# Performance work log

Hardware: AMD Instinct MI355X
Metric: run time of the kernel (lower is better)

Reference implementation:

```python
import jax, jax.numpy as jnp
import numpy as np

ALPHA = 0.8  # LeakyReLU negative slope
OUT_DIM = 128
EDGE_DIM = 64


def setup_inputs() -> dict:
    key = jax.random.key(0)
    ks = jax.random.split(key, 6)
    N, NS, IN, OUT, ED = 25000, 32, 128, OUT_DIM, EDGE_DIM
    return {
        "input": jax.random.normal(ks[0], (N, IN), jnp.float32),
        "neigh_feat": jax.random.normal(ks[1], (N * NS, IN), jnp.float32),
        "edge_emb": jax.random.normal(ks[2], (N * NS, ED), jnp.float32),
        "mask": jnp.zeros((N,), jnp.int32),  # unused by forward, kept for signature fidelity
        "W": jax.random.normal(ks[3], (IN, OUT), jnp.float32) * 0.1,
        "W2": jax.random.normal(ks[4], (IN, OUT), jnp.float32) * 0.1,
        "a": jax.random.normal(ks[5], (2 * OUT + ED, 1), jnp.float32) * 0.1,
    }


def reference(input, neigh_feat, edge_emb, mask, W, W2, a):
    N = input.shape[0]
    ns = neigh_feat.shape[0] // N
    out_dim = W.shape[1]
    ed = edge_emb.shape[1]

    x = input @ W                                   # [N, out]
    neighs = (neigh_feat @ W2).reshape(N, ns, out_dim)  # [N, ns, out]
    edge = edge_emb.reshape(N, ns, ed)              # [N, ns, ed]

    # a_input @ a decomposed: avoid materializing the repeated/concatenated tensor.
    a_x = a[:out_dim, 0]
    a_n = a[out_dim:2 * out_dim, 0]
    a_e = a[2 * out_dim:, 0]
    scores = (x @ a_x)[:, None] + neighs @ a_n + edge @ a_e  # [N, ns]
    e = jnp.where(scores > 0, scores, ALPHA * scores)        # LeakyReLU(alpha)

    attention = jax.nn.softmax(e, axis=1)           # softmax over neighbors
    # dropout p=0.0 (eval) -> identity

    h_prime = jnp.einsum("ns,nsd->nd", attention, neighs)  # [N, out]
    output = jnp.concatenate([x, h_prime], axis=1)          # concat_node
    e_agg = jnp.einsum("ns,nse->ne", attention, edge)       # concat_edge
    output = jnp.concatenate([output, e_agg], axis=1)       # [N, 2*out+ed]
    return jax.nn.elu(output)
```

## Files before the change

kernel.cpp:

```cpp
#include <hip/hip_runtime.h>
#include <hip/hip_bf16.h>
#include <math.h>

typedef __bf16 bf16_t;
typedef __attribute__((ext_vector_type(8))) __bf16 bf16x8;
typedef __attribute__((ext_vector_type(4))) __bf16 bf16x4;
typedef __attribute__((ext_vector_type(4))) float f32x4;

#define NB 2

#define WAVE_BARRIER() do {                                    \
    asm volatile("s_waitcnt lgkmcnt(0)" ::: "memory");         \
    __builtin_amdgcn_s_barrier();                              \
  } while (0)

__global__ __launch_bounds__(256) void pack_weights_kernel(
    const float* __restrict__ W, const float* __restrict__ W2,
    const float* __restrict__ a,
    bf16_t* __restrict__ Wp, bf16_t* __restrict__ W2p,
    float* __restrict__ w2an, float* __restrict__ wax) {
  int idx = blockIdx.x * 256 + threadIdx.x;
  int j  = idx & 7;
  int l  = (idx >> 3) & 63;
  int nt = (idx >> 9) & 7;
  int kt = idx >> 12;
  int k   = kt * 32 + (l >> 4) * 8 + j;
  int col = nt * 16 + (l & 15);
  Wp[idx]  = (bf16_t)W[k * 128 + col];
  W2p[idx] = (bf16_t)W2[k * 128 + col];
  if (blockIdx.x == 0 && threadIdx.x < 128) {
    const float* r = W2 + threadIdx.x * 128;
    float s = 0.f;
    for (int c = 0; c < 128; ++c) s += r[c] * a[128 + c];
    w2an[threadIdx.x] = s;
  }
  if (blockIdx.x == 1 && threadIdx.x < 128) {
    const float* r = W + threadIdx.x * 128;
    float s = 0.f;
    for (int c = 0; c < 128; ++c) s += r[c] * a[c];
    wax[threadIdx.x] = s;
  }
}

__global__ __launch_bounds__(256, 4) void node_kernel(
    const float* __restrict__ input,
    const float* __restrict__ neigh_feat, const float* __restrict__ edge_emb,
    const float* __restrict__ a, const float* __restrict__ w2an,
    const float* __restrict__ wax,
    const bf16_t* __restrict__ Wp, const bf16_t* __restrict__ W2p,
    float* __restrict__ out) {
  const int t = threadIdx.x;
  const int w = t >> 6, l = t & 63;
  const int n0 = blockIdx.x * NB;

  __shared__ __align__(16) bf16_t AxAh[16 * 128];
  __shared__ float Agg[NB][128];
  __shared__ float srow[32], se[32];
  __shared__ __align__(16) f32x4 nag[4][32];
  __shared__ __align__(16) f32x4 eag[4][16];
  __shared__ float sxs[8];

  const int q = l & 31;
  const int h = l >> 5;
  const int p = l & 15;
  const int g = l >> 4;

  const f32x4 wn = *(const f32x4*)(w2an + 4 * q);
  const f32x4 ae = *(const f32x4*)(a + 256 + 4 * p);

  f32x4 nA[4], eA[2], nB[4], eB[2];

#define ISSUE(P, node_) do {                                              \
    const float* nf_ = neigh_feat + (size_t)(node_) * 4096 + 4 * t;       \
    n##P[0] = __builtin_nontemporal_load((const f32x4*)(nf_));            \
    n##P[1] = __builtin_nontemporal_load((const f32x4*)(nf_ + 1024));     \
    n##P[2] = __builtin_nontemporal_load((const f32x4*)(nf_ + 2048));     \
    n##P[3] = __builtin_nontemporal_load((const f32x4*)(nf_ + 3072));     \
    const float* ee_ = edge_emb + (size_t)(node_) * 2048 + 4 * t;         \
    e##P[0] = __builtin_nontemporal_load((const f32x4*)(ee_));            \
    e##P[1] = __builtin_nontemporal_load((const f32x4*)(ee_ + 1024));     \
  } while (0)

  ISSUE(A, n0);
  ISSUE(B, n0 + 1);

  {
    const int r2 = t >> 5;
    const int c0 = 4 * (t & 31);
    f32x4 iv = {0.f, 0.f, 0.f, 0.f};
    if (r2 < NB) iv = *(const f32x4*)(input + (size_t)(n0 + r2) * 128 + c0);
    f32x4 wv = *(const f32x4*)(wax + c0);
    float s = iv[0]*wv[0] + iv[1]*wv[1] + iv[2]*wv[2] + iv[3]*wv[3];
    s += __shfl_xor(s, 1);  s += __shfl_xor(s, 2);  s += __shfl_xor(s, 4);
    s += __shfl_xor(s, 8);  s += __shfl_xor(s, 16);
    if ((l & 31) == 0) sxs[r2] = s;
    bf16x4 b;
#pragma unroll
    for (int j = 0; j < 4; ++j) b[j] = (bf16_t)iv[j];
    const int gg = (t & 31) >> 1;
    *(bf16x4*)(&AxAh[r2 * 128 + ((gg ^ r2) << 3) + 4 * (t & 1)]) = b;
    bf16x4 z = {(bf16_t)0.f, (bf16_t)0.f, (bf16_t)0.f, (bf16_t)0.f};
    *(bf16x4*)(&AxAh[1024 + 4 * t]) = z;
  }
  __syncthreads();

  {
    const int arow = l & 15;
    f32x4 acc0 = {}, acc1 = {};
#pragma unroll
    for (int kt = 0; kt < 4; ++kt) {
      bf16x8 af = *(const bf16x8*)(&AxAh[arow * 128 + ((kt * 32 + (l >> 4) * 8) ^ ((arow & 7) << 3))]);
      bf16x8 b0 = *(const bf16x8*)(&Wp[((kt * 8 + 2 * w) * 64 + l) * 8]);
      bf16x8 b1 = *(const bf16x8*)(&Wp[((kt * 8 + 2 * w + 1) * 64 + l) * 8]);
      acc0 = __builtin_amdgcn_mfma_f32_16x16x32_bf16(af, b0, acc0, 0, 0, 0);
      acc1 = __builtin_amdgcn_mfma_f32_16x16x32_bf16(af, b1, acc1, 0, 0, 0);
    }
    if ((l >> 4) < 2) {
#pragma unroll
      for (int j = 0; j < 4; ++j) {
        int row = (l >> 4) * 4 + j;
        if (row < NB) {
          float v0 = acc0[j];
          v0 = v0 > 0.f ? v0 : __expf(v0) - 1.f;
          __builtin_nontemporal_store(v0, out + (size_t)(n0 + row) * 320 + 2 * w * 16 + (l & 15));
          float v1 = acc1[j];
          v1 = v1 > 0.f ? v1 : __expf(v1) - 1.f;
          __builtin_nontemporal_store(v1, out + (size_t)(n0 + row) * 320 + (2 * w + 1) * 16 + (l & 15));
        }
      }
    }
  }

#define BODY(P, kk) do {                                                  \
    const int node = n0 + (kk);                                           \
    _Pragma("unroll")                                                     \
    for (int j = 0; j < 4; ++j) {                                         \
      float s = n##P[j][0]*wn[0] + n##P[j][1]*wn[1]                       \
              + n##P[j][2]*wn[2] + n##P[j][3]*wn[3];                      \
      s += __shfl_xor(s, 1);  s += __shfl_xor(s, 2);                      \
      s += __shfl_xor(s, 4);  s += __shfl_xor(s, 8);                      \
      s += __shfl_xor(s, 16);                                             \
      if (q == 0) srow[8*j + 2*w + h] = s;                                \
    }                                                                     \
    _Pragma("unroll")                                                     \
    for (int j = 0; j < 2; ++j) {                                         \
      float s = e##P[j][0]*ae[0] + e##P[j][1]*ae[1]                       \
              + e##P[j][2]*ae[2] + e##P[j][3]*ae[3];                      \
      s += __shfl_xor(s, 1);  s += __shfl_xor(s, 2);                      \
      s += __shfl_xor(s, 4);  s += __shfl_xor(s, 8);                      \
      if (p == 0) se[16*j + 4*w + g] = s;                                 \
    }                                                                     \
    WAVE_BARRIER();                                                       \
    float av;                                                             \
    {                                                                     \
      float e0 = srow[q] + se[q] + sxs[kk];                               \
      e0 = e0 > 0.f ? e0 : 0.8f * e0;                                     \
       \
      float pe = __expf(e0);                                              \
      float s2 = pe;                                                      \
      s2 += __shfl_xor(s2, 1);                                            \
      s2 += __shfl_xor(s2, 2);                                            \
      s2 += __shfl_xor(s2, 4);                                            \
      s2 += __shfl_xor(s2, 8);                                            \
      s2 += __shfl_xor(s2, 16);                                           \
      av = pe / s2;                                                       \
    }                                                                     \
    {                                                                     \
      f32x4 pn = {0.f, 0.f, 0.f, 0.f};                                    \
      _Pragma("unroll")                                                   \
      for (int j = 0; j < 4; ++j) {                                       \
        float as = __shfl(av, 8*j + 2*w + h);                             \
        pn += as * n##P[j];                                               \
      }                                                                   \
      pn[0] += __shfl_xor(pn[0], 32);                                     \
      pn[1] += __shfl_xor(pn[1], 32);                                     \
      pn[2] += __shfl_xor(pn[2], 32);                                     \
      pn[3] += __shfl_xor(pn[3], 32);                                     \
      if (h == 0) nag[w][q] = pn;                                         \
      f32x4 pv = {0.f, 0.f, 0.f, 0.f};                                    \
      _Pragma("unroll")                                                   \
      for (int j = 0; j < 2; ++j) {                                       \
        float as = __shfl(av, 16*j + 4*w + g);                            \
        pv += as * e##P[j];                                               \
      }                                                                   \
      pv[0] += __shfl_xor(pv[0], 16);                                     \
      pv[1] += __shfl_xor(pv[1], 16);                                     \
      pv[2] += __shfl_xor(pv[2], 16);                                     \
      pv[3] += __shfl_xor(pv[3], 16);                                     \
      pv[0] += __shfl_xor(pv[0], 32);                                     \
      pv[1] += __shfl_xor(pv[1], 32);                                     \
      pv[2] += __shfl_xor(pv[2], 32);                                     \
      pv[3] += __shfl_xor(pv[3], 32);                                     \
      if (l < 16) eag[w][p] = pv;                                         \
    }                                                                     \
    WAVE_BARRIER();                                                       \
    if (t < 128) {                                                        \
      const float* f = (const float*)nag;                                 \
      Agg[kk][t] = f[t] + f[128 + t] + f[256 + t] + f[384 + t];           \
    } else if (t < 192) {                                                 \
      int c = t - 128;                                                    \
      const float* f = (const float*)eag;                                 \
      float v = f[c] + f[64 + c] + f[128 + c] + f[192 + c];               \
      v = v > 0.f ? v : __expf(v) - 1.f;                                  \
      __builtin_nontemporal_store(v, out + (size_t)node * 320 + 256 + c); \
    }                                                                     \
  } while (0)

  BODY(A, 0);
  BODY(B, 1);
#undef BODY
#undef ISSUE

  __syncthreads();

  {
    const int r2 = t >> 5;
    const int c0 = 4 * (t & 31);
    f32x4 v = {0.f, 0.f, 0.f, 0.f};
    if (r2 < NB) v = *(const f32x4*)(&Agg[r2][c0]);
    bf16x4 b;
#pragma unroll
    for (int j = 0; j < 4; ++j) b[j] = (bf16_t)v[j];
    const int gg = (t & 31) >> 1;
    *(bf16x4*)(&AxAh[r2 * 128 + ((gg ^ r2) << 3) + 4 * (t & 1)]) = b;
  }
  __syncthreads();
  {
    const int arow = l & 15;
    f32x4 acc0 = {}, acc1 = {};
#pragma unroll
    for (int kt = 0; kt < 4; ++kt) {
      bf16x8 af = *(const bf16x8*)(&AxAh[arow * 128 + ((kt * 32 + (l >> 4) * 8) ^ ((arow & 7) << 3))]);
      bf16x8 b0 = *(const bf16x8*)(&W2p[((kt * 8 + 2 * w) * 64 + l) * 8]);
      bf16x8 b1 = *(const bf16x8*)(&W2p[((kt * 8 + 2 * w + 1) * 64 + l) * 8]);
      acc0 = __builtin_amdgcn_mfma_f32_16x16x32_bf16(af, b0, acc0, 0, 0, 0);
      acc1 = __builtin_amdgcn_mfma_f32_16x16x32_bf16(af, b1, acc1, 0, 0, 0);
    }
    if ((l >> 4) < 2) {
#pragma unroll
      for (int j = 0; j < 4; ++j) {
        int row = (l >> 4) * 4 + j;
        if (row < NB) {
          float v0 = acc0[j];
          v0 = v0 > 0.f ? v0 : __expf(v0) - 1.f;
          __builtin_nontemporal_store(v0, out + (size_t)(n0 + row) * 320 + 128 + 2 * w * 16 + (l & 15));
          float v1 = acc1[j];
          v1 = v1 > 0.f ? v1 : __expf(v1) - 1.f;
          __builtin_nontemporal_store(v1, out + (size_t)(n0 + row) * 320 + 128 + (2 * w + 1) * 16 + (l & 15));
        }
      }
    }
  }
}

extern "C" void kernel_launch(void* const* d_in, const int* in_sizes, int n_in,
                              void* d_out, int out_size, void* d_ws, size_t ws_size,
                              hipStream_t stream) {
  const float* input = (const float*)d_in[0];
  const float* neigh = (const float*)d_in[1];
  const float* edge  = (const float*)d_in[2];
  const float* W     = (const float*)d_in[4];
  const float* W2    = (const float*)d_in[5];
  const float* a     = (const float*)d_in[6];
  float* out = (float*)d_out;

  const int N = in_sizes[0] / 128;

  bf16_t* W2p  = (bf16_t*)d_ws;
  bf16_t* Wp   = W2p + 16384;
  float*  w2an = (float*)((char*)d_ws + 65536);
  float*  wax  = (float*)((char*)d_ws + 66048);

  pack_weights_kernel<<<64, 256, 0, stream>>>(W, W2, a, Wp, W2p, w2an, wax);
  node_kernel<<<N / NB, 256, 0, stream>>>(input, neigh, edge, a, w2an, wax,
                                          Wp, W2p, out);
}
```

Baseline: 143.1 us.

## Compute attention scores and aggregations with MFMA via LDS transpose reads

Replaces the shuffle-based dot products for neighbor and edge scores with bf16 MFMA against a weight vector placed in one column. Neighbor and edge features are converted to bf16 and staged in LDS, and the attention-weighted aggregation is done by MFMA using ds_read_b64_tr_b16 transposed reads. The aim is to remove the many cross-lane shuffles and the LDS reduction stage. In exchange it adds LDS traffic and bf16 rounding of the score and aggregation inputs, which lowers accuracy.

```diff
diff --git a/kernel.cpp b/kernel.cpp
--- a/kernel.cpp
+++ b/kernel.cpp
@@ -52,33 +52,60 @@
   const int t = threadIdx.x;
   const int w = t >> 6, l = t & 63;
   const int n0 = blockIdx.x * NB;
+  const int lr = l & 15;
+  const int lg = l >> 4;
+  const int half = w >> 1;
+  const int mt = w & 1;
+  const int mrow = mt * 16 + lr;
 
   __shared__ __align__(16) bf16_t AxAh[16 * 128];
+  __shared__ __align__(16) bf16_t NFs[4096];
+  __shared__ __align__(16) bf16_t Es[2048];
   __shared__ float Agg[NB][128];
-  __shared__ float srow[32], se[32];
-  __shared__ __align__(16) f32x4 nag[4][32];
-  __shared__ __align__(16) f32x4 eag[4][16];
+  __shared__ float srp[2][32], sep[2][32];
   __shared__ float sxs[8];
 
-  const int q = l & 31;
-  const int h = l >> 5;
-  const int p = l & 15;
-  const int g = l >> 4;
-
-  const f32x4 wn = *(const f32x4*)(w2an + 4 * q);
-  const f32x4 ae = *(const f32x4*)(a + 256 + 4 * p);
-
-  f32x4 nA[4], eA[2], nB[4], eB[2];
-
-#define ISSUE(P, node_) do {                                              \
-    const float* nf_ = neigh_feat + (size_t)(node_) * 4096 + 4 * t;       \
-    n##P[0] = __builtin_nontemporal_load((const f32x4*)(nf_));            \
-    n##P[1] = __builtin_nontemporal_load((const f32x4*)(nf_ + 1024));     \
-    n##P[2] = __builtin_nontemporal_load((const f32x4*)(nf_ + 2048));     \
-    n##P[3] = __builtin_nontemporal_load((const f32x4*)(nf_ + 3072));     \
-    const float* ee_ = edge_emb + (size_t)(node_) * 2048 + 4 * t;         \
-    e##P[0] = __builtin_nontemporal_load((const f32x4*)(ee_));            \
-    e##P[1] = __builtin_nontemporal_load((const f32x4*)(ee_ + 1024));     \
+  bf16x8 bw0, bw1, be;
+  {
+    const float* ws = w2an + half * 64 + lg * 8;
+    f32x4 u0 = *(const f32x4*)(ws);
+    f32x4 u1 = *(const f32x4*)(ws + 4);
+    f32x4 u2 = *(const f32x4*)(ws + 32);
+    f32x4 u3 = *(const f32x4*)(ws + 36);
+    const float* es = a + 256 + half * 32 + lg * 8;
+    f32x4 u4 = *(const f32x4*)(es);
+    f32x4 u5 = *(const f32x4*)(es + 4);
+#pragma unroll
+    for (int j = 0; j < 4; ++j) {
+      bw0[j]   = lr == 0 ? (bf16_t)u0[j] : (bf16_t)0.f;
+      bw0[j+4] = lr == 0 ? (bf16_t)u1[j] : (bf16_t)0.f;
+      bw1[j]   = lr == 0 ? (bf16_t)u2[j] : (bf16_t)0.f;
+      bw1[j+4] = lr == 0 ? (bf16_t)u3[j] : (bf16_t)0.f;
+      be[j]    = lr == 0 ? (bf16_t)u4[j] : (bf16_t)0.f;
+      be[j+4]  = lr == 0 ? (bf16_t)u5[j] : (bf16_t)0.f;
+    }
+  }
+
+  const int posm = (((mrow >> 2) & 1) << 2) | (mrow >> 3);
+  const int c0 = half * 64 + lg * 8;
+  const int c1 = c0 + 32;
+  const int ce = half * 32 + lg * 8;
+  const int wr0 = ((c0 >> 4) * 8 + posm) * 64 + (mrow & 3) * 16 + (c0 & 15);
+  const int wr1 = ((c1 >> 4) * 8 + posm) * 64 + (mrow & 3) * 16 + (c1 & 15);
+  const int wre = ((ce >> 4) * 8 + posm) * 64 + (mrow & 3) * 16 + (ce & 15);
+
+  f32x4 sA0, sA1, sA2, sA3, sA4, sA5;
+  f32x4 sB0, sB1, sB2, sB3, sB4, sB5;
+
+#define ISSUE(P, node_) do {                                                   \
+    const float* nf_ = neigh_feat + (size_t)(node_) * 4096 + mrow * 128 + c0;  \
+    s##P##0 = __builtin_nontemporal_load((const f32x4*)(nf_));                 \
+    s##P##1 = __builtin_nontemporal_load((const f32x4*)(nf_ + 4));             \
+    s##P##2 = __builtin_nontemporal_load((const f32x4*)(nf_ + 32));            \
+    s##P##3 = __builtin_nontemporal_load((const f32x4*)(nf_ + 36));            \
+    const float* ee_ = edge_emb + (size_t)(node_) * 2048 + mrow * 64 + ce;     \
+    s##P##4 = __builtin_nontemporal_load((const f32x4*)(ee_));                 \
+    s##P##5 = __builtin_nontemporal_load((const f32x4*)(ee_ + 4));             \
   } while (0)
 
   ISSUE(A, n0);
@@ -86,10 +113,10 @@
 
   {
     const int r2 = t >> 5;
-    const int c0 = 4 * (t & 31);
+    const int c0p = 4 * (t & 31);
     f32x4 iv = {0.f, 0.f, 0.f, 0.f};
-    if (r2 < NB) iv = *(const f32x4*)(input + (size_t)(n0 + r2) * 128 + c0);
-    f32x4 wv = *(const f32x4*)(wax + c0);
+    if (r2 < NB) iv = *(const f32x4*)(input + (size_t)(n0 + r2) * 128 + c0p);
+    f32x4 wv = *(const f32x4*)(wax + c0p);
     float s = iv[0]*wv[0] + iv[1]*wv[1] + iv[2]*wv[2] + iv[3]*wv[3];
     s += __shfl_xor(s, 1);  s += __shfl_xor(s, 2);  s += __shfl_xor(s, 4);
     s += __shfl_xor(s, 8);  s += __shfl_xor(s, 16);
@@ -105,105 +132,109 @@
   __syncthreads();
 
   {
-    const int arow = l & 15;
     f32x4 acc0 = {}, acc1 = {};
 #pragma unroll
     for (int kt = 0; kt < 4; ++kt) {
-      bf16x8 af = *(const bf16x8*)(&AxAh[arow * 128 + ((kt * 32 + (l >> 4) * 8) ^ ((arow & 7) << 3))]);
+      bf16x8 af = *(const bf16x8*)(&AxAh[lr * 128 + ((kt * 32 + lg * 8) ^ ((lr & 7) << 3))]);
       bf16x8 b0 = *(const bf16x8*)(&Wp[((kt * 8 + 2 * w) * 64 + l) * 8]);
       bf16x8 b1 = *(const bf16x8*)(&Wp[((kt * 8 + 2 * w + 1) * 64 + l) * 8]);
       acc0 = __builtin_amdgcn_mfma_f32_16x16x32_bf16(af, b0, acc0, 0, 0, 0);
       acc1 = __builtin_amdgcn_mfma_f32_16x16x32_bf16(af, b1, acc1, 0, 0, 0);
     }
-    if ((l >> 4) < 2) {
+    if (lg < 2) {
 #pragma unroll
       for (int j = 0; j < 4; ++j) {
-        int row = (l >> 4) * 4 + j;
+        int row = lg * 4 + j;
         if (row < NB) {
           float v0 = acc0[j];
           v0 = v0 > 0.f ? v0 : __expf(v0) - 1.f;
-          __builtin_nontemporal_store(v0, out + (size_t)(n0 + row) * 320 + 2 * w * 16 + (l & 15));
+          __builtin_nontemporal_store(v0, out + (size_t)(n0 + row) * 320 + 2 * w * 16 + lr);
           float v1 = acc1[j];
           v1 = v1 > 0.f ? v1 : __expf(v1) - 1.f;
-          __builtin_nontemporal_store(v1, out + (size_t)(n0 + row) * 320 + (2 * w + 1) * 16 + (l & 15));
+          __builtin_nontemporal_store(v1, out + (size_t)(n0 + row) * 320 + (2 * w + 1) * 16 + lr);
         }
       }
     }
   }
 
-#define BODY(P, kk) do {                                                  \
-    const int node = n0 + (kk);                                           \
-    _Pragma("unroll")                                                     \
-    for (int j = 0; j < 4; ++j) {                                         \
-      float s = n##P[j][0]*wn[0] + n##P[j][1]*wn[1]                       \
-              + n##P[j][2]*wn[2] + n##P[j][3]*wn[3];                      \
-      s += __shfl_xor(s, 1);  s += __shfl_xor(s, 2);                      \
-      s += __shfl_xor(s, 4);  s += __shfl_xor(s, 8);                      \
-      s += __shfl_xor(s, 16);                                             \
-      if (q == 0) srow[8*j + 2*w + h] = s;                                \
-    }                                                                     \
-    _Pragma("unroll")                                                     \
-    for (int j = 0; j < 2; ++j) {                                         \
-      float s = e##P[j][0]*ae[0] + e##P[j][1]*ae[1]                       \
-              + e##P[j][2]*ae[2] + e##P[j][3]*ae[3];                      \
-      s += __shfl_xor(s, 1);  s += __shfl_xor(s, 2);                      \
-      s += __shfl_xor(s, 4);  s += __shfl_xor(s, 8);                      \
-      if (p == 0) se[16*j + 4*w + g] = s;                                 \
-    }                                                                     \
-    WAVE_BARRIER();                                                       \
-    float av;                                                             \
-    {                                                                     \
-      float e0 = srow[q] + se[q] + sxs[kk];                               \
-      e0 = e0 > 0.f ? e0 : 0.8f * e0;                                     \
-       \
-      float pe = __expf(e0);                                              \
-      float s2 = pe;                                                      \
-      s2 += __shfl_xor(s2, 1);                                            \
-      s2 += __shfl_xor(s2, 2);                                            \
-      s2 += __shfl_xor(s2, 4);                                            \
-      s2 += __shfl_xor(s2, 8);                                            \
-      s2 += __shfl_xor(s2, 16);                                           \
-      av = pe / s2;                                                       \
-    }                                                                     \
-    {                                                                     \
-      f32x4 pn = {0.f, 0.f, 0.f, 0.f};                                    \
-      _Pragma("unroll")                                                   \
-      for (int j = 0; j < 4; ++j) {                                       \
-        float as = __shfl(av, 8*j + 2*w + h);                             \
-        pn += as * n##P[j];                                               \
-      }                                                                   \
-      pn[0] += __shfl_xor(pn[0], 32);                                     \
-      pn[1] += __shfl_xor(pn[1], 32);                                     \
-      pn[2] += __shfl_xor(pn[2], 32);                                     \
-      pn[3] += __shfl_xor(pn[3], 32);                                     \
-      if (h == 0) nag[w][q] = pn;                                         \
-      f32x4 pv = {0.f, 0.f, 0.f, 0.f};                                    \
-      _Pragma("unroll")                                                   \
-      for (int j = 0; j < 2; ++j) {                                       \
-        float as = __shfl(av, 16*j + 4*w + g);                            \
-        pv += as * e##P[j];                                               \
-      }                                                                   \
-      pv[0] += __shfl_xor(pv[0], 16);                                     \
-      pv[1] += __shfl_xor(pv[1], 16);                                     \
-      pv[2] += __shfl_xor(pv[2], 16);                                     \
-      pv[3] += __shfl_xor(pv[3], 16);                                     \
-      pv[0] += __shfl_xor(pv[0], 32);                                     \
-      pv[1] += __shfl_xor(pv[1], 32);                                     \
-      pv[2] += __shfl_xor(pv[2], 32);                                     \
-      pv[3] += __shfl_xor(pv[3], 32);                                     \
-      if (l < 16) eag[w][p] = pv;                                         \
-    }                                                                     \
-    WAVE_BARRIER();                                                       \
-    if (t < 128) {                                                        \
-      const float* f = (const float*)nag;                                 \
-      Agg[kk][t] = f[t] + f[128 + t] + f[256 + t] + f[384 + t];           \
-    } else if (t < 192) {                                                 \
-      int c = t - 128;                                                    \
-      const float* f = (const float*)eag;                                 \
-      float v = f[c] + f[64 + c] + f[128 + c] + f[192 + c];               \
-      v = v > 0.f ? v : __expf(v) - 1.f;                                  \
-      __builtin_nontemporal_store(v, out + (size_t)node * 320 + 256 + c); \
-    }                                                                     \
+#define BODY(P, kk) do {                                                       \
+    const int node = n0 + (kk);                                                \
+    bf16x8 af0, af1, aef;                                                      \
+    _Pragma("unroll")                                                          \
+    for (int j = 0; j < 4; ++j) {                                              \
+      af0[j] = (bf16_t)s##P##0[j]; af0[j+4] = (bf16_t)s##P##1[j];              \
+      af1[j] = (bf16_t)s##P##2[j]; af1[j+4] = (bf16_t)s##P##3[j];              \
+      aef[j] = (bf16_t)s##P##4[j]; aef[j+4] = (bf16_t)s##P##5[j];              \
+    }                                                                          \
+    *(bf16x8*)(&NFs[wr0]) = af0;                                               \
+    *(bf16x8*)(&NFs[wr1]) = af1;                                               \
+    *(bf16x8*)(&Es[wre])  = aef;                                               \
+    f32x4 accN = {0.f, 0.f, 0.f, 0.f};                                         \
+    accN = __builtin_amdgcn_mfma_f32_16x16x32_bf16(af0, bw0, accN, 0, 0, 0);   \
+    accN = __builtin_amdgcn_mfma_f32_16x16x32_bf16(af1, bw1, accN, 0, 0, 0);   \
+    f32x4 accE = {0.f, 0.f, 0.f, 0.f};                                         \
+    accE = __builtin_amdgcn_mfma_f32_16x16x32_bf16(aef, be, accE, 0, 0, 0);    \
+    if (lr == 0) {                                                             \
+      *(f32x4*)(&srp[half][mt * 16 + lg * 4]) = accN;                          \
+      *(f32x4*)(&sep[half][mt * 16 + lg * 4]) = accE;                          \
+    }                                                                          \
+    WAVE_BARRIER();                                                            \
+    float av;                                                                  \
+    {                                                                          \
+      int q = l & 31;                                                          \
+      float e0 = srp[0][q] + srp[1][q] + sep[0][q] + sep[1][q] + sxs[kk];      \
+      e0 = e0 > 0.f ? e0 : 0.8f * e0;                                          \
+      float pe = __expf(e0);                                                   \
+      float s2 = pe;                                                           \
+      s2 += __shfl_xor(s2, 1);  s2 += __shfl_xor(s2, 2);                       \
+      s2 += __shfl_xor(s2, 4);  s2 += __shfl_xor(s2, 8);                       \
+      s2 += __shfl_xor(s2, 16);                                                \
+      av = pe / s2;                                                            \
+    }                                                                          \
+    bf16x8 att8;                                                               \
+    _Pragma("unroll")                                                          \
+    for (int j = 0; j < 8; ++j) att8[j] = (bf16_t)__shfl(av, lg * 8 + j);      \
+    {                                                                          \
+          \
+      const unsigned lof = 8u * (unsigned)lr + 128u * (unsigned)lg;            \
+      const unsigned nb  = (unsigned)(size_t)(&NFs[0]) + lof;                  \
+      const unsigned eb  = (unsigned)(size_t)(&Es[0]) + lof;                   \
+      _Pragma("unroll")                                                        \
+      for (int ci = 0; ci < 2; ++ci) {                                         \
+        const int cg = 2 * w + ci;                                             \
+        unsigned ad = nb + (unsigned)(cg * 1024);                              \
+        unsigned long long lo, hi;                                             \
+        asm volatile("ds_read_b64_tr_b16 %0, %2\n\t"                           \
+                     "ds_read_b64_tr_b16 %1, %2 offset:512\n\t"                \
+                     "s_waitcnt lgkmcnt(0)"                                    \
+                     : "=&v"(lo), "=&v"(hi) : "v"(ad));                        \
+        bf16x8 bfrag;                                                          \
+        unsigned long long uu[2] = {lo, hi};                                   \
+        __builtin_memcpy(&bfrag, uu, 16);                                      \
+        f32x4 acg = {0.f, 0.f, 0.f, 0.f};                                      \
+        acg = __builtin_amdgcn_mfma_f32_16x16x32_bf16(att8, bfrag, acg, 0,0,0);\
+        if (l < 16) Agg[kk][cg * 16 + lr] = acg[0];                            \
+      }                                                                        \
+      {                                                                        \
+        unsigned ad = eb + (unsigned)(w * 1024);                               \
+        unsigned long long lo, hi;                                             \
+        asm volatile("ds_read_b64_tr_b16 %0, %2\n\t"                           \
+                     "ds_read_b64_tr_b16 %1, %2 offset:512\n\t"                \
+                     "s_waitcnt lgkmcnt(0)"                                    \
+                     : "=&v"(lo), "=&v"(hi) : "v"(ad));                        \
+        bf16x8 bfrag;                                                          \
+        unsigned long long uu[2] = {lo, hi};                                   \
+        __builtin_memcpy(&bfrag, uu, 16);                                      \
+        f32x4 acg = {0.f, 0.f, 0.f, 0.f};                                      \
+        acg = __builtin_amdgcn_mfma_f32_16x16x32_bf16(att8, bfrag, acg, 0,0,0);\
+        if (l < 16) {                                                          \
+          float v = acg[0];                                                    \
+          v = v > 0.f ? v : __expf(v) - 1.f;                                   \
+          __builtin_nontemporal_store(v, out + (size_t)node * 320 + 256 + w * 16 + lr); \
+        }                                                                      \
+      }                                                                        \
+    }                                                                          \
+    WAVE_BARRIER();                                                            \
   } while (0)
 
   BODY(A, 0);
@@ -215,9 +246,9 @@
 
   {
     const int r2 = t >> 5;
-    const int c0 = 4 * (t & 31);
+    const int c0p = 4 * (t & 31);
     f32x4 v = {0.f, 0.f, 0.f, 0.f};
-    if (r2 < NB) v = *(const f32x4*)(&Agg[r2][c0]);
+    if (r2 < NB) v = *(const f32x4*)(&Agg[r2][c0p]);
     bf16x4 b;
 #pragma unroll
     for (int j = 0; j < 4; ++j) b[j] = (bf16_t)v[j];
@@ -226,27 +257,26 @@
   }
   __syncthreads();
   {
-    const int arow = l & 15;
     f32x4 acc0 = {}, acc1 = {};
 #pragma unroll
     for (int kt = 0; kt < 4; ++kt) {
-      bf16x8 af = *(const bf16x8*)(&AxAh[arow * 128 + ((kt * 32 + (l >> 4) * 8) ^ ((arow & 7) << 3))]);
+      bf16x8 af = *(const bf16x8*)(&AxAh[lr * 128 + ((kt * 32 + lg * 8) ^ ((lr & 7) << 3))]);
       bf16x8 b0 = *(const bf16x8*)(&W2p[((kt * 8 + 2 * w) * 64 + l) * 8]);
       bf16x8 b1 = *(const bf16x8*)(&W2p[((kt * 8 + 2 * w + 1) * 64 + l) * 8]);
       acc0 = __builtin_amdgcn_mfma_f32_16x16x32_bf16(af, b0, acc0, 0, 0, 0);
       acc1 = __builtin_amdgcn_mfma_f32_16x16x32_bf16(af, b1, acc1, 0, 0, 0);
     }
-    if ((l >> 4) < 2) {
+    if (lg < 2) {
 #pragma unroll
       for (int j = 0; j < 4; ++j) {
-        int row = (l >> 4) * 4 + j;
+        int row = lg * 4 + j;
         if (row < NB) {
           float v0 = acc0[j];
           v0 = v0 > 0.f ? v0 : __expf(v0) - 1.f;
-          __builtin_nontemporal_store(v0, out + (size_t)(n0 + row) * 320 + 128 + 2 * w * 16 + (l & 15));
+          __builtin_nontemporal_store(v0, out + (size_t)(n0 + row) * 320 + 128 + 2 * w * 16 + lr);
           float v1 = acc1[j];
           v1 = v1 > 0.f ? v1 : __expf(v1) - 1.f;
-          __builtin_nontemporal_store(v1, out + (size_t)(n0 + row) * 320 + 128 + (2 * w + 1) * 16 + (l & 15));
+          __builtin_nontemporal_store(v1, out + (size_t)(n0 + row) * 320 + 128 + (2 * w + 1) * 16 + lr);
         }
       }
     }
```

Measured after the change: 175.3 us. +22.5%, slower.
